# Optimization experiments

Hardware: AMD Instinct MI355X
Metric: run time of the kernel (lower is better)

Reference implementation:

```python
import jax, jax.numpy as jnp
import numpy as np

DIM = 1024
NUM_HEADS = 16
BATCH = 4
SEQ = 2048
SCALE = (DIM // NUM_HEADS) ** -0.5
MASK_VAL = -10000000.0


def setup_inputs() -> dict:
    key = jax.random.key(0)
    k1, k2, k3, k4 = jax.random.split(key, 4)
    inputs = jax.random.normal(k1, (BATCH, SEQ, DIM), dtype=jnp.float32)
    # xavier-ish scaling for weights
    W_qkv = jax.random.normal(k2, (3 * DIM, DIM), dtype=jnp.float32) * (1.0 / np.sqrt(DIM))
    W_fc = jax.random.normal(k3, (DIM, DIM), dtype=jnp.float32) * (1.0 / np.sqrt(DIM))
    b_fc = jnp.zeros((DIM,), dtype=jnp.float32)
    padding_mask = jax.random.randint(k4, (BATCH, SEQ), 0, 2, dtype=jnp.int32)
    return {"inputs": inputs, "W_qkv": W_qkv, "W_fc": W_fc, "b_fc": b_fc,
            "padding_mask": padding_mask}


def reference(inputs, W_qkv, W_fc, b_fc, padding_mask):
    B, N, C = inputs.shape
    H = NUM_HEADS
    Dh = C // H
    # qkv projection (torch Linear: x @ W.T), [B,N,3C]
    qkv = jnp.einsum('bnc,oc->bno', inputs, W_qkv)
    qkv = qkv.reshape(B, N, 3, H, Dh).transpose(2, 0, 3, 1, 4)  # [3,B,H,N,Dh]
    q, k, v = qkv[0], qkv[1], qkv[2]
    att = jnp.einsum('bhqd,bhkd->bhqk', q, k) * SCALE  # [B,H,N,N]
    mask = padding_mask[:, None, None, :]              # [B,1,1,N]
    att = jnp.where(mask > 0, jnp.float32(MASK_VAL), att)
    att = jax.nn.softmax(att, axis=-1)
    x = jnp.einsum('bhqk,bhkd->bhqd', att, v)          # [B,H,N,Dh]
    x = x.transpose(0, 2, 1, 3).reshape(B, N, C)       # [B,N,C]
    out = jnp.einsum('bnc,oc->bno', x, W_fc) + b_fc
    return out
```

## Files before the change

kernel.cpp:

```cpp
#include <hip/hip_runtime.h>
#include <stdint.h>

constexpr int kDim  = 1024;
constexpr int kH    = 16;
constexpr int kB    = 4;
constexpr int kSeq  = 2048;
constexpr int kDh   = 64;
constexpr int kMTot = kB * kSeq;
constexpr int kNQkv = 3 * kDim;
constexpr float kScale = 0.125f;
constexpr float kLog2e = 1.44269504088896f;
constexpr float kC1    = kScale * kLog2e;
constexpr float kMaxSub = 10.0f;
constexpr float kMk2Un   = -kMaxSub * kLog2e;
constexpr float kMk2Mask = -1.0e9f;
constexpr int kPld = 72;
constexpr int kCld = 136;

typedef __attribute__((ext_vector_type(8))) short short8;
typedef __attribute__((ext_vector_type(4))) float floatx4;

__device__ __forceinline__ unsigned short f2bf(float f) {
  union { float f; unsigned u; } v; v.f = f;
  unsigned r = v.u + 0x7fffu + ((v.u >> 16) & 1u);
  return (unsigned short)(r >> 16);
}
__device__ __forceinline__ unsigned short f2bf_fast(float f) {
  union { float f; unsigned u; } v; v.f = f;
  return (unsigned short)((v.u + 0x8000u) >> 16);
}
__device__ __forceinline__ float vexp2(float x) {
  float r; asm("v_exp_f32 %0, %1" : "=v"(r) : "v"(x)); return r;
}
__device__ __forceinline__ void gl2lds16(const void* g, void* l) {
  __builtin_amdgcn_global_load_lds(
      (const __attribute__((address_space(1))) unsigned int*)g,
      (__attribute__((address_space(3))) unsigned int*)l, 16, 0, 0);
}

__global__ void __launch_bounds__(256) cvt_scan(
    const float4* __restrict__ x, const float4* __restrict__ wq,
    const float4* __restrict__ wf,
    ushort4* __restrict__ xb, ushort4* __restrict__ wqb, ushort4* __restrict__ wfb,
    const int* __restrict__ pm, int* __restrict__ cidx, int* __restrict__ nkd,
    int* __restrict__ ctr) {
  const int X4  = (kMTot * kDim) / 4;
  const int WQ4 = (kNQkv * kDim) / 4;
  const int NCVT = 12288;
  if (blockIdx.x >= NCVT) {
    const int b = blockIdx.x - NCVT;
    const int t = threadIdx.x;
    const int lane = t & 63, wv = t >> 6;
    __shared__ int wsum[4];
    __shared__ int woff[5];
    if (b == 0 && t == 0) *ctr = 256;
    int base = t * 8;
    int keep[8]; int cnt = 0;
#pragma unroll
    for (int j = 0; j < 8; j++) {
      keep[j] = (pm[b * kSeq + base + j] <= 0) ? 1 : 0;
      cnt += keep[j];
    }
    int pre = cnt;
#pragma unroll
    for (int off = 1; off < 64; off <<= 1) {
      int v = __shfl_up(pre, off, 64);
      if (lane >= off) pre += v;
    }
    int excl = pre - cnt;
    if (lane == 63) wsum[wv] = pre;
    __syncthreads();
    if (t == 0) {
      int s = 0;
#pragma unroll
      for (int w = 0; w < 4; w++) { woff[w] = s; s += wsum[w]; }
      woff[4] = s;
      nkd[b] = s;
    }
    __syncthreads();
    const int nk = woff[4];
    int kp = woff[wv] + excl;
#pragma unroll
    for (int j = 0; j < 8; j++) {
      int n = base + j;
      int pos = keep[j] ? kp : nk + (n - kp);
      cidx[b * kSeq + pos] = b * kSeq + n;
      kp += keep[j];
    }
    return;
  }
  int i = blockIdx.x * 256 + threadIdx.x;
  float4 v; ushort4* dst;
  if (i < X4)            { v = x[i];             dst = xb  + i; }
  else if (i < X4 + WQ4) { v = wq[i - X4];       dst = wqb + (i - X4); }
  else                   { v = wf[i - X4 - WQ4]; dst = wfb + (i - X4 - WQ4); }
  ushort4 o;
  o.x = f2bf(v.x); o.y = f2bf(v.y); o.z = f2bf(v.z); o.w = f2bf(v.w);
  *dst = o;
}

__global__ void __launch_bounds__(512, 2) gemm_qkv(
    const unsigned short* __restrict__ xb, const unsigned short* __restrict__ wqb,
    const int* __restrict__ cidx, const int* __restrict__ nkd,
    int* __restrict__ ctr,
    unsigned short* __restrict__ qb, unsigned short* __restrict__ kb,
    unsigned short* __restrict__ vtb) {
  extern __shared__ __attribute__((aligned(16))) unsigned short smem[];
  __shared__ int s_slot;
  unsigned short* As0 = smem;
  unsigned short* Bs0 = smem + 16384;
  unsigned short* As1 = smem + 32768;
  unsigned short* Bs1 = smem + 49152;

  const int t = threadIdx.x;
  const int lane = t & 63, wv = t >> 6;
  const int wm = (wv >> 2) << 7;
  const int wn = (wv & 3) << 6;
  const int lrow = lane & 15, quad = lane >> 4, l7 = lane & 7;
  const int srow = t >> 3;
  const int pu8 = (t & 7) * 8;
  const int lu8 = ((t & 7) ^ (srow & 7)) * 8;
  const int off0 = (quad ^ l7) * 8;

  const int rr0 = (nkd[0] + 127) >> 7, rr1 = (nkd[1] + 127) >> 7;
  const int rr2 = (nkd[2] + 127) >> 7, rr3 = (nkd[3] + 127) >> 7;
  const int tb0 = (rr0 + 1) >> 1, tb1 = (rr1 + 1) >> 1;
  const int tb2 = (rr2 + 1) >> 1, tb3 = (rr3 + 1) >> 1;
  const int pA = tb0, pB = pA + tb1, pC = pB + tb2, pD = pC + tb3;
  const int NT = 128 + 8 * pD;

#define STAGE_B(buf, p, k0) gl2lds16(brow + (int64_t)(p) * 64 * kDim + (k0), \
                                     (buf) + ((p) * 64 + srow) * 64 + pu8)
#define STAGE_A(buf, p, k0) gl2lds16(arow[p] + (k0), \
                                     (buf) + ((p) * 64 + srow) * 64 + pu8)
#define BARRIER() { asm volatile("" ::: "memory"); \
                    __builtin_amdgcn_s_barrier(); \
                    asm volatile("" ::: "memory"); }
#define LDA(q) { \
    const unsigned short* Ar0_ = Ac + (wm + (2*(q)) * 16 + lrow) * 64; \
    const unsigned short* Ar1_ = Ac + (wm + (2*(q)+1) * 16 + lrow) * 64; \
    af00 = *(const short8*)(Ar0_ + off0); \
    af01 = *(const short8*)(Ar0_ + (off0 ^ 32)); \
    af10 = *(const short8*)(Ar1_ + off0); \
    af11 = *(const short8*)(Ar1_ + (off0 ^ 32)); }
#define MFMAQ(q) { \
    __builtin_amdgcn_s_setprio(1); \
    _Pragma("unroll") \
    for (int ni = 0; ni < 4; ni++) { \
      acc[2*(q)][ni]   = __builtin_amdgcn_mfma_f32_16x16x32_bf16(af00, bfr[ni][0], acc[2*(q)][ni],   0, 0, 0); \
      acc[2*(q)+1][ni] = __builtin_amdgcn_mfma_f32_16x16x32_bf16(af10, bfr[ni][0], acc[2*(q)+1][ni], 0, 0, 0); \
    } \
    _Pragma("unroll") \
    for (int ni = 0; ni < 4; ni++) { \
      acc[2*(q)][ni]   = __builtin_amdgcn_mfma_f32_16x16x32_bf16(af01, bfr[ni][1], acc[2*(q)][ni],   0, 0, 0); \
      acc[2*(q)+1][ni] = __builtin_amdgcn_mfma_f32_16x16x32_bf16(af11, bfr[ni][1], acc[2*(q)+1][ni], 0, 0, 0); \
    } \
    __builtin_amdgcn_s_setprio(0); }

  int slot = blockIdx.x;
  while (slot < NT) {
    int which, tN, tMl, bb, rbv;
    if (slot < 128) {
      which = 0; tN = (slot & 3) * 256;
      int tMg = (slot >> 2) * 256;
      bb = tMg >> 11; tMl = tMg & 2047; rbv = 16;
    } else {
      int id = slot - 128;
      const int TK = 4 * pD;
      which = (id < TK) ? 1 : 2;
      if (which == 2) id -= TK;
      int col = id & 3, j = id >> 2;
      int pj;
      if (j < pA)      { bb = 0; pj = j;      rbv = rr0; }
      else if (j < pB) { bb = 1; pj = j - pA; rbv = rr1; }
      else if (j < pC) { bb = 2; pj = j - pB; rbv = rr2; }
      else             { bb = 3; pj = j - pC; rbv = rr3; }
      tMl = pj * 256;
      tN = (which == 1 ? 1024 : 2048) + col * 256;
    }
    int nrows;
    if (which == 0) nrows = 256;
    else { int rem = rbv * 128 - tMl; nrows = (rem >= 256) ? 256 : 128; }
    const bool na4 = (nrows == 256);
    const bool act = (wm < nrows);
    const bool vblk = (which == 2);

    const unsigned short* arow[4];
#pragma unroll
    for (int p = 0; p < 4; p++) {
      int pe = (!na4 && p > 1) ? 1 : p;
      int rl = tMl + pe * 64 + srow;
      int rid = (which == 0) ? (bb * 2048 + rl) : cidx[bb * 2048 + rl];
      arow[p] = xb + (int64_t)rid * kDim + lu8;
    }
    const unsigned short* brow = wqb + (int64_t)(tN + srow) * kDim + lu8;

    floatx4 acc[8][4];
    floatx4 zero = {0.f, 0.f, 0.f, 0.f};
#pragma unroll
    for (int mi = 0; mi < 8; mi++)
#pragma unroll
      for (int ni = 0; ni < 4; ni++) acc[mi][ni] = zero;

    STAGE_B(Bs0, 0, 0); STAGE_B(Bs0, 1, 0); STAGE_B(Bs0, 2, 0); STAGE_B(Bs0, 3, 0);
    STAGE_A(As0, 0, 0);
    if (na4) STAGE_A(As0, 2, 0);
    STAGE_A(As0, 1, 0);
    if (na4) STAGE_A(As0, 3, 0);
    STAGE_B(Bs1, 0, 64); STAGE_B(Bs1, 1, 64); STAGE_B(Bs1, 2, 64); STAGE_B(Bs1, 3, 64);
    if (na4) { asm volatile("s_waitcnt vmcnt(6)" ::: "memory"); }
    else     { asm volatile("s_waitcnt vmcnt(5)" ::: "memory"); }
    BARRIER();

    for (int tt = 0; tt < 16; ++tt) {
      unsigned short* Ac = (tt & 1) ? As1 : As0;
      unsigned short* Bc = (tt & 1) ? Bs1 : Bs0;
      unsigned short* An = (tt & 1) ? As0 : As1;
      const int kn  = (tt + 1) * 64;
      const int kn2 = (tt + 2) * 64;
      const bool stA = (tt < 15);
      const bool stB = (tt < 14);

      short8 bfr[4][2];
      short8 af00, af01, af10, af11;

      if (act) {
#pragma unroll
        for (int ni = 0; ni < 4; ni++) {
          const unsigned short* Br_ = Bc + (wn + ni * 16 + lrow) * 64;
          bfr[ni][0] = *(const short8*)(Br_ + off0);
          bfr[ni][1] = *(const short8*)(Br_ + (off0 ^ 32));
        }
        LDA(0);
      }
      if (stA) { STAGE_A(An, 0, kn); if (na4) STAGE_A(An, 2, kn); }
      BARRIER();
      if (act) MFMAQ(0);
      BARRIER();
      if (act) LDA(1);
      if (stA) { STAGE_A(An, 1, kn); if (na4) STAGE_A(An, 3, kn); }
      BARRIER();
      if (act) MFMAQ(1);
      if (stA) {
        if (na4) { asm volatile("s_waitcnt vmcnt(8)" ::: "memory"); }
        else     { asm volatile("s_waitcnt vmcnt(6)" ::: "memory"); }
      } else {
        asm volatile("s_waitcnt vmcnt(0)" ::: "memory");
      }
      BARRIER();
      if (act) LDA(2);
      if (stB) { STAGE_B(Bc, 0, kn2); STAGE_B(Bc, 1, kn2); }
      BARRIER();
      if (act) MFMAQ(2);
      BARRIER();
      if (act) LDA(3);
      if (stB) { STAGE_B(Bc, 2, kn2); STAGE_B(Bc, 3, kn2); }
      BARRIER();
      if (act) MFMAQ(3);
      if (stB)      { if (na4) { asm volatile("s_waitcnt vmcnt(6)" ::: "memory"); }
                      else     { asm volatile("s_waitcnt vmcnt(5)" ::: "memory"); } }
      else if (stA) { if (na4) { asm volatile("s_waitcnt vmcnt(2)" ::: "memory"); }
                      else     { asm volatile("s_waitcnt vmcnt(1)" ::: "memory"); } }
      else          { asm volatile("s_waitcnt vmcnt(0)" ::: "memory"); }
      BARRIER();
    }

    unsigned short* Cs = smem;
    const int h4 = (tN >> 6) & 15;
#pragma unroll
    for (int h = 0; h < 2; h++) {
      const bool writer = ((((wv & 3) >> 1) == h) && act);
      const int cwn = (wv & 1) * 64;
      if (!vblk) {
        if (writer) {
#pragma unroll
          for (int mi = 0; mi < 8; mi++)
#pragma unroll
            for (int ni = 0; ni < 4; ni++)
#pragma unroll
              for (int r = 0; r < 4; r++) {
                int row = wm + mi * 16 + quad * 4 + r;
                int c = cwn + ni * 16 + lrow;
                Cs[row * kCld + c] = f2bf(acc[mi][ni][r]);
              }
        }
        asm volatile("s_waitcnt lgkmcnt(0)" ::: "memory");
        BARRIER();
        unsigned short* qk = (which == 0) ? qb : kb;
        const int itn = nrows >> 6;
#pragma unroll
        for (int g = 0; g < 2; g++) {
          int hh = (h4 + h * 2 + g) & 15;
          unsigned short* base = qk + ((int64_t)((bb << 4) + hh) << 17)
                                 + (int64_t)tMl * 64;
          for (int it = 0; it < itn; it++) {
            int off = it * 4096 + t * 8;
            int n = off >> 6;
            int d = off & 63;
            *(short8*)(base + off) = *(const short8*)(Cs + n * kCld + g * 64 + d);
          }
        }
        BARRIER();
      } else {
        if (writer) {
#pragma unroll
          for (int mi = 0; mi < 8; mi++)
#pragma unroll
            for (int ni = 0; ni < 4; ni++)
#pragma unroll
              for (int r = 0; r < 4; r++) {
                int row = wm + mi * 16 + quad * 4 + r;
                int c = cwn + ni * 16 + lrow;
                Cs[c * 264 + row] = f2bf(acc[mi][ni][r]);
              }
        }
        asm volatile("s_waitcnt lgkmcnt(0)" ::: "memory");
        BARRIER();
        const int c8n = nrows >> 3;
#pragma unroll
        for (int g = 0; g < 2; g++) {
          int hh = (h4 + h * 2 + g) & 15;
          unsigned short* vbase = vtb + (((int64_t)((bb << 4) + hh)) << 17) + tMl;
#pragma unroll
          for (int it = 0; it < 4; it++) {
            int off = it * 512 + t;
            int d = off >> 5, c8 = off & 31;
            if (c8 < c8n)
              *(short8*)(vbase + (int64_t)d * 2048 + c8 * 8) =
                  *(const short8*)(Cs + (g * 64 + d) * 264 + c8 * 8);
          }
        }
        BARRIER();
      }
    }

    if (t == 0) s_slot = atomicAdd(ctr, 1);
    __syncthreads();
    slot = s_slot;
  }
#undef STAGE_B
#undef STAGE_A
#undef LDA
#undef MFMAQ
#undef BARRIER
}

__global__ void __launch_bounds__(256, 4) attn(
    const unsigned short* __restrict__ qb, const unsigned short* __restrict__ kb,
    const unsigned short* __restrict__ vtb, const int* __restrict__ nkd,
    unsigned short* __restrict__ xab) {
  __shared__ __attribute__((aligned(16))) unsigned short Ks[64 * 64];
  __shared__ __attribute__((aligned(16))) unsigned short Vs[64 * 64];
  __shared__ __attribute__((aligned(16))) unsigned short Ps[4][2][16 * kPld];

  const int t = threadIdx.x, lane = t & 63, wv = t >> 6;
  const int lrow = lane & 15, quad = lane >> 4, l7 = lane & 7;
  const int qblk = blockIdx.x & 15, bh = blockIdx.x >> 4;
  const int b = bh >> 4, h = bh & 15;
  const int q0 = qblk * 128;
  const int srow = t >> 3;
  const int pu8 = (t & 7) * 8;
  const int lu8 = ((t & 7) ^ (srow & 7)) * 8;
  const int off0 = (quad ^ l7) * 8;

  const int nk  = nkd[b];
  const int nkt = (nk + 63) >> 6;

  const unsigned short* Qb0 = qb + ((int64_t)bh * kSeq + q0 + wv * 16 + lrow) * kDh;
  short8 qf[2][2];
  qf[0][0] = *(const short8*)(Qb0 + quad * 8);
  qf[0][1] = *(const short8*)(Qb0 + 32 + quad * 8);
  qf[1][0] = *(const short8*)(Qb0 + 64 * kDh + quad * 8);
  qf[1][1] = *(const short8*)(Qb0 + 64 * kDh + 32 + quad * 8);

  float l_run[2][4];
  floatx4 o_acc[2][4];
  floatx4 zero = {0.f, 0.f, 0.f, 0.f};
#pragma unroll
  for (int t2 = 0; t2 < 2; t2++) {
#pragma unroll
    for (int r = 0; r < 4; r++) l_run[t2][r] = 0.f;
#pragma unroll
    for (int di = 0; di < 4; di++) o_acc[t2][di] = zero;
  }

  const unsigned short* Kbase = kb  + (int64_t)bh * kSeq * kDh;
  const unsigned short* Vbase = vtb + (int64_t)bh * kDh * kSeq;

  for (int kt = 0; kt < nkt; ++kt) {
    const int k0 = kt * 64;
    {
      int r0 = srow, r1 = srow + 32;
      gl2lds16(Kbase + (int64_t)(k0 + r0) * kDh + lu8, Ks + r0 * 64 + pu8);
      gl2lds16(Kbase + (int64_t)(k0 + r1) * kDh + lu8, Ks + r1 * 64 + pu8);
      gl2lds16(Vbase + (int64_t)r0 * kSeq + k0 + lu8,  Vs + r0 * 64 + pu8);
      gl2lds16(Vbase + (int64_t)r1 * kSeq + k0 + lu8,  Vs + r1 * 64 + pu8);
    }
    __syncthreads();

    floatx4 s[2][4];
#pragma unroll
    for (int ni = 0; ni < 4; ni++) {
      const unsigned short* Kr = Ks + (ni * 16 + lrow) * 64;
      short8 kf0 = *(const short8*)(Kr + off0);
      short8 kf1 = *(const short8*)(Kr + (off0 ^ 32));
#pragma unroll
      for (int t2 = 0; t2 < 2; t2++) {
        floatx4 tmp = __builtin_amdgcn_mfma_f32_16x16x32_bf16(qf[t2][0], kf0, zero, 0, 0, 0);
        s[t2][ni]   = __builtin_amdgcn_mfma_f32_16x16x32_bf16(qf[t2][1], kf1, tmp, 0, 0, 0);
      }
    }
    float mk2[4];
#pragma unroll
    for (int c = 0; c < 4; c++)
      mk2[c] = (k0 + c * 16 + lrow < nk) ? kMk2Un : kMk2Mask;

#pragma unroll
    for (int t2 = 0; t2 < 2; t2++) {
      unsigned short* Pw = &Ps[wv][t2][0];
#pragma unroll
      for (int r = 0; r < 4; r++) {
        int prow = (quad * 4 + r) * kPld + lrow;
#pragma unroll
        for (int c = 0; c < 4; c++) {
          float p = vexp2(fmaf(s[t2][c][r], kC1, mk2[c]));
          l_run[t2][r] += p;
          Pw[prow + c * 16] = f2bf_fast(p);
        }
      }
    }
    asm volatile("s_waitcnt lgkmcnt(0)" ::: "memory");

#pragma unroll
    for (int ks = 0; ks < 2; ks++) {
      short8 pf0 = *(const short8*)(&Ps[wv][0][0] + lrow * kPld + ks * 32 + quad * 8);
      short8 pf1 = *(const short8*)(&Ps[wv][1][0] + lrow * kPld + ks * 32 + quad * 8);
      const int voff = off0 ^ (ks * 32);
#pragma unroll
      for (int di = 0; di < 4; di++) {
        short8 vf = *(const short8*)(Vs + (di * 16 + lrow) * 64 + voff);
        o_acc[0][di] = __builtin_amdgcn_mfma_f32_16x16x32_bf16(pf0, vf, o_acc[0][di], 0, 0, 0);
        o_acc[1][di] = __builtin_amdgcn_mfma_f32_16x16x32_bf16(pf1, vf, o_acc[1][di], 0, 0, 0);
      }
    }
    __syncthreads();
  }

#pragma unroll
  for (int t2 = 0; t2 < 2; t2++) {
#pragma unroll
    for (int r = 0; r < 4; r++) {
      float l = l_run[t2][r];
      l += __shfl_xor(l, 1, 64);
      l += __shfl_xor(l, 2, 64);
      l += __shfl_xor(l, 4, 64);
      l += __shfl_xor(l, 8, 64);
      float inv = 1.0f / l;
      int n = q0 + t2 * 64 + wv * 16 + quad * 4 + r;
      int64_t rowbase = ((int64_t)b * kSeq + n) * kDim + h * kDh;
#pragma unroll
      for (int di = 0; di < 4; di++)
        xab[rowbase + di * 16 + lrow] = f2bf(o_acc[t2][di][r] * inv);
    }
  }
}

__global__ void __launch_bounds__(256) gemm_fc(
    const unsigned short* __restrict__ xab, const unsigned short* __restrict__ wfb,
    const float* __restrict__ bfc, float* __restrict__ out) {
  __shared__ __attribute__((aligned(16))) unsigned short As[128 * 64];
  __shared__ __attribute__((aligned(16))) unsigned short Bs[128 * 64];
  const int tN = blockIdx.x * 128, tM = blockIdx.y * 128;
  const int t = threadIdx.x;
  const int lane = t & 63, wv = t >> 6;
  const int wm = (wv >> 1) << 6, wn = (wv & 1) << 6;
  const int lrow = lane & 15, quad = lane >> 4, l7 = lane & 7;
  const int srow = t >> 3;
  const int pu8 = (t & 7) * 8;
  const int lu8 = ((t & 7) ^ (srow & 7)) * 8;
  const int off0 = (quad ^ l7) * 8;

  floatx4 acc[4][4];
  floatx4 zero = {0.f, 0.f, 0.f, 0.f};
#pragma unroll
  for (int mi = 0; mi < 4; mi++)
#pragma unroll
    for (int ni = 0; ni < 4; ni++) acc[mi][ni] = zero;

  for (int k0 = 0; k0 < kDim; k0 += 64) {
#pragma unroll
    for (int p = 0; p < 4; ++p) {
      int r = srow + p * 32;
      gl2lds16(xab + (int64_t)(tM + r) * kDim + k0 + lu8, As + r * 64 + pu8);
      gl2lds16(wfb + (int64_t)(tN + r) * kDim + k0 + lu8, Bs + r * 64 + pu8);
    }
    __syncthreads();
#pragma unroll
    for (int kk = 0; kk < 64; kk += 32) {
      short8 af[4], bf[4];
#pragma unroll
      for (int mi = 0; mi < 4; mi++)
        af[mi] = *(const short8*)(As + (wm + mi * 16 + lrow) * 64 + (off0 ^ kk));
#pragma unroll
      for (int ni = 0; ni < 4; ni++)
        bf[ni] = *(const short8*)(Bs + (wn + ni * 16 + lrow) * 64 + (off0 ^ kk));
#pragma unroll
      for (int mi = 0; mi < 4; mi++)
#pragma unroll
        for (int ni = 0; ni < 4; ni++)
          acc[mi][ni] = __builtin_amdgcn_mfma_f32_16x16x32_bf16(af[mi], bf[ni], acc[mi][ni], 0, 0, 0);
    }
    __syncthreads();
  }

#pragma unroll
  for (int ni = 0; ni < 4; ni++) {
    int o = tN + wn + ni * 16 + lrow;
    float bias = bfc[o];
#pragma unroll
    for (int mi = 0; mi < 4; mi++) {
#pragma unroll
      for (int r = 0; r < 4; r++) {
        int i = tM + wm + mi * 16 + quad * 4 + r;
        out[(int64_t)i * kDim + o] = acc[mi][ni][r] + bias;
      }
    }
  }
}

extern "C" void kernel_launch(void* const* d_in, const int* in_sizes, int n_in,
                              void* d_out, int out_size, void* d_ws, size_t ws_size,
                              hipStream_t stream) {
  (void)in_sizes; (void)n_in; (void)out_size; (void)ws_size;
  const float* x    = (const float*)d_in[0];
  const float* wqkv = (const float*)d_in[1];
  const float* wfc  = (const float*)d_in[2];
  const float* bfc  = (const float*)d_in[3];
  const int*   pm   = (const int*)d_in[4];
  float* out = (float*)d_out;

  char* ws = (char*)d_ws;
  unsigned short* xb  = (unsigned short*)(ws);
  unsigned short* wqb = (unsigned short*)(ws + 16777216);
  unsigned short* wfb = (unsigned short*)(ws + 23068672);
  unsigned short* qb  = (unsigned short*)(ws + 25165824);
  unsigned short* kb  = (unsigned short*)(ws + 41943040);
  unsigned short* vtb = (unsigned short*)(ws + 58720256);
  int*            cidx= (int*)(ws + 75497472);
  int*            nkd = (int*)(ws + 75530240);
  int*            ctr = (int*)(ws + 75530256);
  unsigned short* xab = xb;

  static bool s_attr_set = false;
  if (!s_attr_set) {
    (void)hipFuncSetAttribute((const void*)gemm_qkv,
                              hipFuncAttributeMaxDynamicSharedMemorySize, 131072);
    s_attr_set = true;
  }

  cvt_scan<<<12288 + kB, 256, 0, stream>>>(
      (const float4*)x, (const float4*)wqkv, (const float4*)wfc,
      (ushort4*)xb, (ushort4*)wqb, (ushort4*)wfb, pm, cidx, nkd, ctr);
  gemm_qkv<<<256, 512, 131072, stream>>>(
      xb, wqb, cidx, nkd, ctr, qb, kb, vtb);
  attn<<<kB * kH * (kSeq / 128), 256, 0, stream>>>(qb, kb, vtb, nkd, xab);
  gemm_fc<<<dim3(kDim / 128, kMTot / 128), 256, 0, stream>>>(xab, wfb, bfc, out);
}
```

Measured before the change: 237.5 us.

## Simplify QKV GEMM main loop to single-stage double-buffered prefetch

Replaces the four-phase interleaved K-loop with a plain double-buffered scheme. Both the first and second K-tiles are now prestaged, each later iteration issues all A/B loads for the next tile up front, and the MFMAs for the current tile run over two 32-wide K halves. The old version staged B two tiles ahead, split the work with several barriers and partial vmcnt waits, and raised wave priority around the MFMA bursts; all of that is dropped for one full vmcnt(0) wait and a single barrier per tile. This cuts barrier count and scheduling complexity, but the prefetch distance is shorter and holding eight A fragments at once raises register pressure.

```diff
diff --git a/kernel.cpp b/kernel.cpp
--- a/kernel.cpp
+++ b/kernel.cpp
@@ -136,26 +136,6 @@
 #define BARRIER() { asm volatile("" ::: "memory"); \
                     __builtin_amdgcn_s_barrier(); \
                     asm volatile("" ::: "memory"); }
-#define LDA(q) { \
-    const unsigned short* Ar0_ = Ac + (wm + (2*(q)) * 16 + lrow) * 64; \
-    const unsigned short* Ar1_ = Ac + (wm + (2*(q)+1) * 16 + lrow) * 64; \
-    af00 = *(const short8*)(Ar0_ + off0); \
-    af01 = *(const short8*)(Ar0_ + (off0 ^ 32)); \
-    af10 = *(const short8*)(Ar1_ + off0); \
-    af11 = *(const short8*)(Ar1_ + (off0 ^ 32)); }
-#define MFMAQ(q) { \
-    __builtin_amdgcn_s_setprio(1); \
-    _Pragma("unroll") \
-    for (int ni = 0; ni < 4; ni++) { \
-      acc[2*(q)][ni]   = __builtin_amdgcn_mfma_f32_16x16x32_bf16(af00, bfr[ni][0], acc[2*(q)][ni],   0, 0, 0); \
-      acc[2*(q)+1][ni] = __builtin_amdgcn_mfma_f32_16x16x32_bf16(af10, bfr[ni][0], acc[2*(q)+1][ni], 0, 0, 0); \
-    } \
-    _Pragma("unroll") \
-    for (int ni = 0; ni < 4; ni++) { \
-      acc[2*(q)][ni]   = __builtin_amdgcn_mfma_f32_16x16x32_bf16(af01, bfr[ni][1], acc[2*(q)][ni],   0, 0, 0); \
-      acc[2*(q)+1][ni] = __builtin_amdgcn_mfma_f32_16x16x32_bf16(af11, bfr[ni][1], acc[2*(q)+1][ni], 0, 0, 0); \
-    } \
-    __builtin_amdgcn_s_setprio(0); }
 
   int slot = blockIdx.x;
   while (slot < NT) {
@@ -203,65 +183,47 @@
       for (int ni = 0; ni < 4; ni++) acc[mi][ni] = zero;
 
     STAGE_B(Bs0, 0, 0); STAGE_B(Bs0, 1, 0); STAGE_B(Bs0, 2, 0); STAGE_B(Bs0, 3, 0);
-    STAGE_A(As0, 0, 0);
-    if (na4) STAGE_A(As0, 2, 0);
-    STAGE_A(As0, 1, 0);
-    if (na4) STAGE_A(As0, 3, 0);
+    STAGE_A(As0, 0, 0); STAGE_A(As0, 1, 0);
+    if (na4) { STAGE_A(As0, 2, 0); STAGE_A(As0, 3, 0); }
     STAGE_B(Bs1, 0, 64); STAGE_B(Bs1, 1, 64); STAGE_B(Bs1, 2, 64); STAGE_B(Bs1, 3, 64);
-    if (na4) { asm volatile("s_waitcnt vmcnt(6)" ::: "memory"); }
-    else     { asm volatile("s_waitcnt vmcnt(5)" ::: "memory"); }
+    STAGE_A(As1, 0, 64); STAGE_A(As1, 1, 64);
+    if (na4) { STAGE_A(As1, 2, 64); STAGE_A(As1, 3, 64); }
+    if (na4) { asm volatile("s_waitcnt vmcnt(8)" ::: "memory"); }
+    else     { asm volatile("s_waitcnt vmcnt(6)" ::: "memory"); }
     BARRIER();
 
     for (int tt = 0; tt < 16; ++tt) {
-      unsigned short* Ac = (tt & 1) ? As1 : As0;
-      unsigned short* Bc = (tt & 1) ? Bs1 : Bs0;
+      const unsigned short* Ac = (tt & 1) ? As1 : As0;
+      const unsigned short* Bc = (tt & 1) ? Bs1 : Bs0;
       unsigned short* An = (tt & 1) ? As0 : As1;
-      const int kn  = (tt + 1) * 64;
-      const int kn2 = (tt + 2) * 64;
-      const bool stA = (tt < 15);
-      const bool stB = (tt < 14);
-
-      short8 bfr[4][2];
-      short8 af00, af01, af10, af11;
+      unsigned short* Bn = (tt & 1) ? Bs0 : Bs1;
+
+      if (tt >= 1 && tt < 15) {
+        const int kn = (tt + 1) * 64;
+        STAGE_B(Bn, 0, kn); STAGE_B(Bn, 1, kn); STAGE_B(Bn, 2, kn); STAGE_B(Bn, 3, kn);
+        STAGE_A(An, 0, kn); STAGE_A(An, 1, kn);
+        if (na4) { STAGE_A(An, 2, kn); STAGE_A(An, 3, kn); }
+      }
 
       if (act) {
 #pragma unroll
-        for (int ni = 0; ni < 4; ni++) {
-          const unsigned short* Br_ = Bc + (wn + ni * 16 + lrow) * 64;
-          bfr[ni][0] = *(const short8*)(Br_ + off0);
-          bfr[ni][1] = *(const short8*)(Br_ + (off0 ^ 32));
+        for (int kk = 0; kk < 64; kk += 32) {
+          short8 bf[4], af[8];
+#pragma unroll
+          for (int ni = 0; ni < 4; ni++)
+            bf[ni] = *(const short8*)(Bc + (wn + ni * 16 + lrow) * 64 + (off0 ^ kk));
+#pragma unroll
+          for (int mi = 0; mi < 8; mi++)
+            af[mi] = *(const short8*)(Ac + (wm + mi * 16 + lrow) * 64 + (off0 ^ kk));
+#pragma unroll
+          for (int mi = 0; mi < 8; mi++)
+#pragma unroll
+            for (int ni = 0; ni < 4; ni++)
+              acc[mi][ni] = __builtin_amdgcn_mfma_f32_16x16x32_bf16(af[mi], bf[ni], acc[mi][ni], 0, 0, 0);
         }
-        LDA(0);
-      }
-      if (stA) { STAGE_A(An, 0, kn); if (na4) STAGE_A(An, 2, kn); }
-      BARRIER();
-      if (act) MFMAQ(0);
-      BARRIER();
-      if (act) LDA(1);
-      if (stA) { STAGE_A(An, 1, kn); if (na4) STAGE_A(An, 3, kn); }
-      BARRIER();
-      if (act) MFMAQ(1);
-      if (stA) {
-        if (na4) { asm volatile("s_waitcnt vmcnt(8)" ::: "memory"); }
-        else     { asm volatile("s_waitcnt vmcnt(6)" ::: "memory"); }
-      } else {
-        asm volatile("s_waitcnt vmcnt(0)" ::: "memory");
-      }
-      BARRIER();
-      if (act) LDA(2);
-      if (stB) { STAGE_B(Bc, 0, kn2); STAGE_B(Bc, 1, kn2); }
-      BARRIER();
-      if (act) MFMAQ(2);
-      BARRIER();
-      if (act) LDA(3);
-      if (stB) { STAGE_B(Bc, 2, kn2); STAGE_B(Bc, 3, kn2); }
-      BARRIER();
-      if (act) MFMAQ(3);
-      if (stB)      { if (na4) { asm volatile("s_waitcnt vmcnt(6)" ::: "memory"); }
-                      else     { asm volatile("s_waitcnt vmcnt(5)" ::: "memory"); } }
-      else if (stA) { if (na4) { asm volatile("s_waitcnt vmcnt(2)" ::: "memory"); }
-                      else     { asm volatile("s_waitcnt vmcnt(1)" ::: "memory"); } }
-      else          { asm volatile("s_waitcnt vmcnt(0)" ::: "memory"); }
+      }
+
+      asm volatile("s_waitcnt vmcnt(0)" ::: "memory");
       BARRIER();
     }
 
@@ -340,8 +302,6 @@
   }
 #undef STAGE_B
 #undef STAGE_A
-#undef LDA
-#undef MFMAQ
 #undef BARRIER
 }
 
```

After: 228.8 us (median of 2 runs). 1.04x faster.
